# Performance work log

Measured on AMD Instinct MI355X. Metric: run time of the kernel, lower is better.

The kernel has to match this reference:

```python
import jax, jax.numpy as jnp
import numpy as np

B, N, C, Q, H, RATIO = 8, 8700, 256, 300, 8, 4
D = C // H
HID = C * RATIO
EPS = 1e-5


def _ln(x, w, b):
    m = jnp.mean(x, axis=-1, keepdims=True)
    v = jnp.mean((x - m) ** 2, axis=-1, keepdims=True)
    return (x - m) * jax.lax.rsqrt(v + EPS) * w + b


def setup_inputs() -> dict:
    key = jax.random.key(0)
    ks = jax.random.split(key, 8)
    s = 0.02
    return {
        "x": jax.random.normal(ks[0], (B, N, C), jnp.float32),
        # linear weights stored [in, out] (y = x @ W), no biases (qkv_bias=False, Mlp bias=False)
        "Wq": jax.random.normal(ks[1], (C, C), jnp.float32) * s,
        "Wk": jax.random.normal(ks[2], (C, C), jnp.float32) * s,
        "Wv": jax.random.normal(ks[3], (C, C), jnp.float32) * s,
        "Wp": jax.random.normal(ks[4], (C, C), jnp.float32) * s,
        "W1": jax.random.normal(ks[5], (C, HID), jnp.float32) * s,
        "W2": jax.random.normal(ks[6], (HID, C), jnp.float32) * s,
        "ln1_w": jnp.ones((C,), jnp.float32),
        "ln1_b": jnp.zeros((C,), jnp.float32),
        "ln2_w": jnp.ones((C,), jnp.float32),
        "ln2_b": jnp.zeros((C,), jnp.float32),
        "gamma1": jnp.ones((C,), jnp.float32),
        "gamma2": jnp.ones((C,), jnp.float32),
    }


def reference(x, Wq, Wk, Wv, Wp, W1, W2, ln1_w, ln1_b, ln2_w, ln2_b, gamma1, gamma2):
    scale = D ** -0.5
    xn = _ln(x, ln1_w, ln1_b)                       # [B,N,C]
    # SAQAttn: queries only from the first Q tokens; keys/values from all N tokens
    q = (xn[:, :Q] @ Wq).reshape(B, Q, H, D) * scale  # [B,Q,H,D]
    k = (xn @ Wk).reshape(B, N, H, D)
    v = (xn @ Wv).reshape(B, N, H, D)
    attn = jax.nn.softmax(jnp.einsum('bqhd,bnhd->bhqn', q, k), axis=-1)  # [B,H,Q,N]
    x_det = jnp.einsum('bhqn,bnhd->bqhd', attn, v).reshape(B, Q, C) @ Wp  # [B,Q,C]
    # residual with layer-scale gamma1; context tokens pass normed features through
    x_attn = jnp.concatenate([x_det, xn[:, Q:]], axis=1)
    x = x + gamma1 * x_attn
    # tokens_norm=False: norm2 only on query tokens
    x = jnp.concatenate([_ln(x[:, :Q], ln2_w, ln2_b), x[:, Q:]], axis=1)
    # MLP on query tokens with layer-scale gamma2 (exact GELU, as nn.GELU default)
    det = gamma2 * (jax.nn.gelu(x[:, :Q] @ W1, approximate=False) @ W2)
    # faithful to source: x_res + cat([det, x[:,Q:]]) doubles the context tokens
    return x + jnp.concatenate([det, x[:, Q:]], axis=1)
```

## Files before the change

kernel.cpp:

```cpp
#include <hip/hip_runtime.h>

#define BB 8
#define NN 8700
#define CC 256
#define QQ 300
#define HH 8
#define DD 32
#define HIDN 1024
#define NSPLIT 16
#define TSTR (NSPLIT * 64)
#define KSLACK 1536

typedef unsigned short u16;
typedef __attribute__((ext_vector_type(8))) short short8;
typedef __attribute__((ext_vector_type(4))) float f32x4;

#define MFMA16(a, b, c) __builtin_amdgcn_mfma_f32_16x16x32_bf16((a), (b), (c), 0, 0, 0)

__device__ __forceinline__ unsigned int cvtpk(float lo, float hi) {
    unsigned int r;
    asm("v_cvt_pk_bf16_f32 %0, %1, %2" : "=v"(r) : "v"(lo), "v"(hi));
    return r;
}
__device__ __forceinline__ u16 f2b_hw(float f) { return (u16)cvtpk(f, 0.f); }
__device__ __forceinline__ float b2f(u16 u) {
    unsigned int x = ((unsigned int)u) << 16;
    return __builtin_bit_cast(float, x);
}
__device__ __forceinline__ void gload16(const u16* g, u16* l) {
    __builtin_amdgcn_global_load_lds(
        (const __attribute__((address_space(1))) void*)g,
        (__attribute__((address_space(3))) void*)l, 16, 0, 0);
}

__global__ __launch_bounds__(256)
void wprep_t(const float* __restrict__ Wq, const float* __restrict__ Wk,
             const float* __restrict__ Wv, const float* __restrict__ Wp,
             const float* __restrict__ W1, const float* __restrict__ W2,
             u16* __restrict__ dst, float qscale)
{
    __shared__ u16 tl[64][66];
    int bid = blockIdx.x;
    const float* src; int K, N, tr, tc; size_t dof; float sc = 1.f;
    if (bid < 64) {
        int mat = bid >> 4, ti = bid & 15;
        src = (mat == 0) ? Wq : (mat == 1) ? Wk : (mat == 2) ? Wv : Wp;
        K = 256; N = 256; tr = ti >> 2; tc = ti & 3;
        dof = (size_t)mat * 65536;
        if (mat == 0) sc = qscale;
    } else if (bid < 128) {
        int ti = bid - 64; src = W1; K = 256; N = 1024; tr = ti >> 4; tc = ti & 15; dof = 262144;
    } else {
        int ti = bid - 128; src = W2; K = 1024; N = 256; tr = ti >> 2; tc = ti & 3; dof = 524288;
    }
    int tid = threadIdx.x;
    int jj = tid & 63;
    int i0 = tid >> 6;
#pragma unroll
    for (int ii = 0; ii < 16; ii++) {
        int kk = i0 * 16 + ii;
        float v = src[(size_t)(tr * 64 + kk) * N + tc * 64 + jj] * sc;
        tl[kk][jj] = f2b_hw(v);
    }
    __syncthreads();
#pragma unroll
    for (int ii = 0; ii < 16; ii++) {
        int nn = i0 * 16 + ii;
        dst[dof + (size_t)(tc * 64 + nn) * K + tr * 64 + jj] = tl[jj][nn];
    }
}

__global__ __launch_bounds__(256)
void ln1_k(const float* __restrict__ x, const float* __restrict__ w,
           const float* __restrict__ bv, const float* __restrict__ g1,
           u16* __restrict__ xn, float* __restrict__ out)
{
    int row = blockIdx.x * 4 + (threadIdx.x >> 6);
    int l = threadIdx.x & 63;
    size_t base = (size_t)row * CC + l * 4;
    float4 xv = *reinterpret_cast<const float4*>(x + base);
    float s  = xv.x + xv.y + xv.z + xv.w;
    float s2 = xv.x * xv.x + xv.y * xv.y + xv.z * xv.z + xv.w * xv.w;
#pragma unroll
    for (int m = 1; m < 64; m <<= 1) {
        s  += __shfl_xor(s,  m, 64);
        s2 += __shfl_xor(s2, m, 64);
    }
    float mean = s * (1.0f / CC);
    float rs = rsqrtf(s2 * (1.0f / CC) - mean * mean + 1e-5f);
    float4 wv = *reinterpret_cast<const float4*>(w  + l * 4);
    float4 bb = *reinterpret_cast<const float4*>(bv + l * 4);
    float n0 = (xv.x - mean) * rs * wv.x + bb.x;
    float n1 = (xv.y - mean) * rs * wv.y + bb.y;
    float n2 = (xv.z - mean) * rs * wv.z + bb.z;
    float n3 = (xv.w - mean) * rs * wv.w + bb.w;
    uint2 u; u.x = cvtpk(n0, n1); u.y = cvtpk(n2, n3);
    *reinterpret_cast<uint2*>(xn + base) = u;
    int n = row % NN;
    if (n >= QQ) {
        float4 gv = *reinterpret_cast<const float4*>(g1 + l * 4);
        float4 o;
        o.x = 2.0f * (xv.x + gv.x * n0);
        o.y = 2.0f * (xv.y + gv.y * n1);
        o.z = 2.0f * (xv.z + gv.z * n2);
        o.w = 2.0f * (xv.w + gv.w * n3);
        *reinterpret_cast<float4*>(out + base) = o;
    }
}

__global__ __launch_bounds__(256)
void ln2_k(const float* __restrict__ x, const float* __restrict__ pd,
           const float* __restrict__ g1, const float* __restrict__ w,
           const float* __restrict__ bv, float* __restrict__ xqf, u16* __restrict__ xqb)
{
    int r = blockIdx.x * 4 + (threadIdx.x >> 6);
    int l = threadIdx.x & 63;
    int b = r / QQ, n = r - b * QQ;
    size_t xoff = ((size_t)b * NN + n) * CC + l * 4;
    size_t roff = (size_t)r * CC + l * 4;
    float4 xv = *reinterpret_cast<const float4*>(x + xoff);
    float4 pv = *reinterpret_cast<const float4*>(pd + roff);
    float4 gv = *reinterpret_cast<const float4*>(g1 + l * 4);
    float x0 = xv.x + gv.x * pv.x;
    float x1 = xv.y + gv.y * pv.y;
    float x2 = xv.z + gv.z * pv.z;
    float x3 = xv.w + gv.w * pv.w;
    float s  = x0 + x1 + x2 + x3;
    float s2 = x0 * x0 + x1 * x1 + x2 * x2 + x3 * x3;
#pragma unroll
    for (int m = 1; m < 64; m <<= 1) {
        s  += __shfl_xor(s,  m, 64);
        s2 += __shfl_xor(s2, m, 64);
    }
    float mean = s * (1.0f / CC);
    float rs = rsqrtf(s2 * (1.0f / CC) - mean * mean + 1e-5f);
    float4 wv = *reinterpret_cast<const float4*>(w  + l * 4);
    float4 bb = *reinterpret_cast<const float4*>(bv + l * 4);
    float n0 = (x0 - mean) * rs * wv.x + bb.x;
    float n1 = (x1 - mean) * rs * wv.y + bb.y;
    float n2 = (x2 - mean) * rs * wv.z + bb.z;
    float n3 = (x3 - mean) * rs * wv.w + bb.w;
    float4 o; o.x = n0; o.y = n1; o.z = n2; o.w = n3;
    *reinterpret_cast<float4*>(xqf + roff) = o;
    uint2 u; u.x = cvtpk(n0, n1); u.y = cvtpk(n2, n3);
    *reinterpret_cast<uint2*>(xqb + roff) = u;
}

__global__ __launch_bounds__(512)
void gemm_kv(const u16* __restrict__ A, const u16* __restrict__ WT,
             u16* __restrict__ Cb, u16* __restrict__ Cb2, int M)
{
    __shared__ u16 alds[64 * 256];
    const int tid = threadIdx.x;
    const int w = tid >> 6, l = tid & 63;
    const int l15 = l & 15, kg = l >> 4;
    const int rowbase = blockIdx.x * 64;
    const f32x4 fz = {0.f, 0.f, 0.f, 0.f};

    {
        const char* gb = (const char*)(A + (size_t)rowbase * CC);
        char* lb = (char*)alds;
#pragma unroll
        for (int j = 0; j < 4; j++) {
            int o = tid * 64 + j * 16;
            short8 v = *reinterpret_cast<const short8*>(gb + o);
            int d = o ^ (((o >> 9) & 7) << 4);
            *reinterpret_cast<short8*>(lb + d) = v;
        }
    }
    __syncthreads();

    const int colbase = w * 64;
    const u16* bp[4];
#pragma unroll
    for (int ni = 0; ni < 4; ni++)
        bp[ni] = WT + (size_t)(colbase + ni * 16 + l15) * CC + kg * 8;

    f32x4 acc[4][4];
#pragma unroll
    for (int mi = 0; mi < 4; mi++)
#pragma unroll
        for (int ni = 0; ni < 4; ni++) acc[mi][ni] = fz;

    const char* lb = (const char*)alds;
    const int sw = (l15 & 7) << 4;
    int abase[4];
#pragma unroll
    for (int mi = 0; mi < 4; mi++) abase[mi] = (mi * 16 + l15) << 9;

#pragma unroll
    for (int ks = 0; ks < 8; ks++) {
        const int koff = ((ks * 64) + (kg * 16)) ^ sw;
        short8 a[4], bfr[4];
#pragma unroll
        for (int mi = 0; mi < 4; mi++)
            a[mi] = *reinterpret_cast<const short8*>(lb + abase[mi] + koff);
#pragma unroll
        for (int ni = 0; ni < 4; ni++)
            bfr[ni] = *reinterpret_cast<const short8*>(bp[ni] + ks * 32);
#pragma unroll
        for (int mi = 0; mi < 4; mi++)
#pragma unroll
            for (int ni = 0; ni < 4; ni++)
                acc[mi][ni] = MFMA16(bfr[ni], a[mi], acc[mi][ni]);
    }

#pragma unroll
    for (int mi = 0; mi < 4; mi++) {
        int r = rowbase + mi * 16 + l15;
        if (r >= M) continue;
#pragma unroll
        for (int ni = 0; ni < 4; ni++) {
            int col0 = colbase + ni * 16 + kg * 4;
            f32x4 v = acc[mi][ni];
            uint2 pk; pk.x = cvtpk(v[0], v[1]); pk.y = cvtpk(v[2], v[3]);
            if (col0 < CC) *reinterpret_cast<uint2*>(Cb  + (size_t)r * CC + col0)        = pk;
            else           *reinterpret_cast<uint2*>(Cb2 + (size_t)r * CC + (col0 - CC)) = pk;
        }
    }
}

template<int EPI, int MT>
__global__ __launch_bounds__(256)
void gemm_k(const u16* __restrict__ A, const u16* __restrict__ WT,
            u16* __restrict__ Cb, u16* __restrict__ Cb2, float* __restrict__ Cf,
            const float* __restrict__ basep, const float* __restrict__ gvec,
            float* __restrict__ outp,
            int M, int K, int ldC, int rpb, int bstr)
{
    constexpr int NM = MT / 16;
    const int w = threadIdx.x >> 6, l = threadIdx.x & 63;
    const int l15 = l & 15, kg = l >> 4;
    const int rowbase = blockIdx.x * MT;
    const int colbase = blockIdx.y * 256 + w * 64;
    const short8 z8 = {0, 0, 0, 0, 0, 0, 0, 0};
    const f32x4 fz = {0.f, 0.f, 0.f, 0.f};

    const u16* ap[NM]; bool av[NM];
#pragma unroll
    for (int mi = 0; mi < NM; mi++) {
        int r = rowbase + mi * 16 + l15;
        av[mi] = (r < M);
        int rr = av[mi] ? r : 0;
        size_t ar = (size_t)(rr / rpb) * bstr + (rr % rpb);
        ap[mi] = A + ar * K + kg * 8;
    }
    const u16* bp[4];
#pragma unroll
    for (int ni = 0; ni < 4; ni++) {
        int col = colbase + ni * 16 + l15;
        bp[ni] = WT + (size_t)col * K + kg * 8;
    }
    f32x4 acc[NM][4];
#pragma unroll
    for (int mi = 0; mi < NM; mi++)
#pragma unroll
        for (int ni = 0; ni < 4; ni++) acc[mi][ni] = fz;

    for (int ks = 0; ks < K; ks += 32) {
        short8 a[NM], bfr[4];
#pragma unroll
        for (int mi = 0; mi < NM; mi++)
            a[mi] = av[mi] ? *reinterpret_cast<const short8*>(ap[mi] + ks) : z8;
#pragma unroll
        for (int ni = 0; ni < 4; ni++)
            bfr[ni] = *reinterpret_cast<const short8*>(bp[ni] + ks);
#pragma unroll
        for (int mi = 0; mi < NM; mi++)
#pragma unroll
            for (int ni = 0; ni < 4; ni++)
                acc[mi][ni] = MFMA16(bfr[ni], a[mi], acc[mi][ni]);
    }
#pragma unroll
    for (int mi = 0; mi < NM; mi++) {
        int r = rowbase + mi * 16 + l15;
        if (r >= M) continue;
#pragma unroll
        for (int ni = 0; ni < 4; ni++) {
            int col0 = colbase + ni * 16 + kg * 4;
            f32x4 v = acc[mi][ni];
            if (EPI == 0) {
                uint2 pk; pk.x = cvtpk(v[0], v[1]); pk.y = cvtpk(v[2], v[3]);
                if (col0 < CC) *reinterpret_cast<uint2*>(Cb  + (size_t)r * ldC + col0)        = pk;
                else           *reinterpret_cast<uint2*>(Cb2 + (size_t)r * ldC + (col0 - CC)) = pk;
            } else if (EPI == 1) {
                float g0 = 0.5f * v[0] * (1.0f + erff(v[0] * 0.70710678118654752f));
                float g1 = 0.5f * v[1] * (1.0f + erff(v[1] * 0.70710678118654752f));
                float g2 = 0.5f * v[2] * (1.0f + erff(v[2] * 0.70710678118654752f));
                float g3 = 0.5f * v[3] * (1.0f + erff(v[3] * 0.70710678118654752f));
                uint2 pk; pk.x = cvtpk(g0, g1); pk.y = cvtpk(g2, g3);
                *reinterpret_cast<uint2*>(Cb + (size_t)r * ldC + col0) = pk;
            } else if (EPI == 2) {
                float4 o; o.x = v[0]; o.y = v[1]; o.z = v[2]; o.w = v[3];
                *reinterpret_cast<float4*>(Cf + (size_t)r * ldC + col0) = o;
            } else {
                float4 xv = *reinterpret_cast<const float4*>(basep + (size_t)r * CC + col0);
                float4 gv = *reinterpret_cast<const float4*>(gvec + col0);
                float4 o;
                o.x = xv.x + gv.x * v[0];
                o.y = xv.y + gv.y * v[1];
                o.z = xv.z + gv.z * v[2];
                o.w = xv.w + gv.w * v[3];
                size_t orow = (size_t)(r / QQ) * NN + (r % QQ);
                *reinterpret_cast<float4*>(outp + orow * CC + col0) = o;
            }
        }
    }
}

__global__ __launch_bounds__(256)
void attn_k(const u16* __restrict__ qm, const u16* __restrict__ km,
            const u16* __restrict__ vm, u16* __restrict__ Opb,
            float* __restrict__ lp)
{
    __shared__ u16 klds[2][64 * 32];
    __shared__ u16 vt[2][32 * 64];
    __shared__ u16 plds[4][2][16 * 64];

    const int bx = blockIdx.x;
    const int split = bx >> 6;
    const int rem = bx & 63;
    const int h = rem >> 3, b = rem & 7;
    const int bh = b * HH + h;
    const int tid = threadIdx.x;
    const int w = tid >> 6, l = tid & 63;
    const int l15 = l & 15, kg = l >> 4;
    const int tstart = split * 64;
    const int nt = (NN - tstart + TSTR - 1) / TSTR;

    const f32x4 fz = {0.f, 0.f, 0.f, 0.f};
    const short os = (short)0x3F80;
    const short8 ones = {os, os, os, os, os, os, os, os};

    const u16* kbase = km + (size_t)b * NN * CC + h * DD;
    const u16* vbase = vm + (size_t)b * NN * CC + h * DD;
    const int vkp = (tid & 31) * 2;
    const int vdg = (tid >> 5) * 4;

    const int krow  = (w << 4) + (l >> 2);
    const int kslot = (l & 3) ^ ((krow >> 1) & 3);
    const u16* ksrc = kbase + (size_t)krow * CC + kslot * 8;

    short8 qfr[5];
#pragma unroll
    for (int qf = 0; qf < 5; qf++) {
        int qrow = w * 80 + qf * 16 + l15;
        int qc = qrow < QQ ? qrow : 0;
        qfr[qf] = *reinterpret_cast<const short8*>(qm + ((size_t)(b * QQ + qc) * CC + h * DD + kg * 8));
    }

    f32x4 o[2][5]; float lpart[5];
#pragma unroll
    for (int qf = 0; qf < 5; qf++) { o[0][qf] = fz; o[1][qf] = fz; lpart[qf] = 0.f; }

    gload16(ksrc + (size_t)tstart * CC, (u16*)((char*)klds[0] + (w << 10)));
    ushort4 v0r = *reinterpret_cast<const ushort4*>(vbase + (size_t)(tstart + vkp) * CC + vdg);
    ushort4 v1r = *reinterpret_cast<const ushort4*>(vbase + (size_t)(tstart + vkp + 1) * CC + vdg);

    char* pl = (char*)plds[w];
    const int rdswz = ((l15 << 7) ^ ((l15 & 7) << 4)) + (kg << 4);
    const int wrbase = (l15 << 7) ^ ((l15 & 7) << 4);

    for (int t = 0; t < nt; ++t) {
        const int n0 = tstart + t * TSTR;
        char* vtb = (char*)vt[t & 1];
#pragma unroll
        for (int i = 0; i < 4; i++) {
            int row = vdg + i;
            unsigned int pk2 = (unsigned int)v0r[i] | ((unsigned int)v1r[i] << 16);
            int byteo = ((row << 7) + (vkp << 1)) ^ ((row & 7) << 4);
            *reinterpret_cast<unsigned int*>(vtb + byteo) = pk2;
        }
        __syncthreads();

        gload16(ksrc + (size_t)(n0 + TSTR) * CC, (u16*)((char*)klds[(t + 1) & 1] + (w << 10)));
        ushort4 v0n = *reinterpret_cast<const ushort4*>(vbase + (size_t)(n0 + TSTR + vkp) * CC + vdg);
        ushort4 v1n = *reinterpret_cast<const ushort4*>(vbase + (size_t)(n0 + TSTR + vkp + 1) * CC + vdg);

        short8 kf[4];
        { const char* klb = (const char*)klds[t & 1];
#pragma unroll
          for (int kb = 0; kb < 4; kb++) {
              int row = kb * 16 + l15;
              int off = (row << 6) + ((kg ^ ((row >> 1) & 3)) << 4);
              kf[kb] = *reinterpret_cast<const short8*>(klb + off);
          } }

        short8 va[2][2];
#pragma unroll
        for (int ks = 0; ks < 2; ks++)
#pragma unroll
            for (int dg = 0; dg < 2; dg++) {
                int row = dg * 16 + l15;
                int byteo = ((row << 7) + 64 * ks + 16 * kg) ^ ((row & 7) << 4);
                va[ks][dg] = *reinterpret_cast<const short8*>(vtb + byteo);
            }

        const bool tail = (n0 + 64 > NN);

#pragma unroll
        for (int qf = 0; qf < 5; qf++) {
            short8 bp0, bp1;
            if (qf > 0) {
                const char* plr = pl + (((qf - 1) & 1) << 11);
                bp0 = *reinterpret_cast<const short8*>(plr + rdswz);
                bp1 = *reinterpret_cast<const short8*>(plr + rdswz + 64);
            }
            f32x4 s[4];
            __builtin_amdgcn_s_setprio(1);
#pragma unroll
            for (int kb = 0; kb < 4; kb++)
                s[kb] = MFMA16(kf[kb], qfr[qf], fz);
            __builtin_amdgcn_s_setprio(0);
            char* plw = pl + ((qf & 1) << 11);
#pragma unroll
            for (int kb = 0; kb < 4; kb++) {
                float p0 = exp2f(s[kb][0]);
                float p1 = exp2f(s[kb][1]);
                float p2 = exp2f(s[kb][2]);
                float p3 = exp2f(s[kb][3]);
                if (tail) {
                    int kbase2 = n0 + 16 * kb + 4 * kg;
                    if (kbase2 + 0 >= NN) p0 = 0.f;
                    if (kbase2 + 1 >= NN) p1 = 0.f;
                    if (kbase2 + 2 >= NN) p2 = 0.f;
                    if (kbase2 + 3 >= NN) p3 = 0.f;
                }
                uint2 pw; pw.x = cvtpk(p0, p1); pw.y = cvtpk(p2, p3);
                *reinterpret_cast<uint2*>(plw + (wrbase + ((16 * kb + 4 * kg) << 1))) = pw;
            }
            if (qf > 0) {
                __builtin_amdgcn_s_setprio(1);
                o[0][qf - 1] = MFMA16(va[0][0], bp0, o[0][qf - 1]);
                o[1][qf - 1] = MFMA16(va[0][1], bp0, o[1][qf - 1]);
                o[0][qf - 1] = MFMA16(va[1][0], bp1, o[0][qf - 1]);
                o[1][qf - 1] = MFMA16(va[1][1], bp1, o[1][qf - 1]);
                f32x4 tsum = MFMA16(ones, bp0, fz);
                tsum = MFMA16(ones, bp1, tsum);
                __builtin_amdgcn_s_setprio(0);
                lpart[qf - 1] += tsum[0];
            }
        }
        {
            const char* plr = pl + 0;
            short8 bp0 = *reinterpret_cast<const short8*>(plr + rdswz);
            short8 bp1 = *reinterpret_cast<const short8*>(plr + rdswz + 64);
            __builtin_amdgcn_s_setprio(1);
            o[0][4] = MFMA16(va[0][0], bp0, o[0][4]);
            o[1][4] = MFMA16(va[0][1], bp0, o[1][4]);
            o[0][4] = MFMA16(va[1][0], bp1, o[0][4]);
            o[1][4] = MFMA16(va[1][1], bp1, o[1][4]);
            f32x4 tsum = MFMA16(ones, bp0, fz);
            tsum = MFMA16(ones, bp1, tsum);
            __builtin_amdgcn_s_setprio(0);
            lpart[4] += tsum[0];
        }
        v0r = v0n; v1r = v1n;
    }

    size_t pb = (size_t)(split * 64 + bh) * QQ;
#pragma unroll
    for (int qf = 0; qf < 5; qf++) {
        int q = w * 80 + qf * 16 + l15;
        if (q >= QQ) continue;
        size_t pr = pb + q;
        if (kg == 0) lp[pr] = lpart[qf];
        uint2 w0; w0.x = cvtpk(o[0][qf][0], o[0][qf][1]); w0.y = cvtpk(o[0][qf][2], o[0][qf][3]);
        uint2 w1; w1.x = cvtpk(o[1][qf][0], o[1][qf][1]); w1.y = cvtpk(o[1][qf][2], o[1][qf][3]);
        *reinterpret_cast<uint2*>(Opb + pr * DD + kg * 4)      = w0;
        *reinterpret_cast<uint2*>(Opb + pr * DD + 16 + kg * 4) = w1;
    }
}

__global__ __launch_bounds__(256)
void comb_k(const u16* __restrict__ Opb, const float* __restrict__ lp, u16* __restrict__ ao)
{
    int g = blockIdx.x * 256 + threadIdx.x;
    int d4 = (g & 7) * 4;
    int row = g >> 3;
    int bh = row / QQ, qq = row - bh * QQ;
    int b = bh >> 3, h = bh & 7;
    float L = 0.f, a0 = 0.f, a1 = 0.f, a2 = 0.f, a3 = 0.f;
#pragma unroll
    for (int s = 0; s < NSPLIT; s++) {
        size_t pr = (size_t)(s * 64 + bh) * QQ + qq;
        L += lp[pr];
        ushort4 ov = *reinterpret_cast<const ushort4*>(Opb + pr * DD + d4);
        a0 += b2f(ov.x); a1 += b2f(ov.y); a2 += b2f(ov.z); a3 += b2f(ov.w);
    }
    float inv = 1.0f / L;
    uint2 u; u.x = cvtpk(a0 * inv, a1 * inv); u.y = cvtpk(a2 * inv, a3 * inv);
    *reinterpret_cast<uint2*>(ao + ((size_t)(b * QQ + qq) * CC + h * DD + d4)) = u;
}

extern "C" void kernel_launch(void* const* d_in, const int* in_sizes, int n_in,
                              void* d_out, int out_size, void* d_ws, size_t ws_size,
                              hipStream_t stream)
{
    (void)in_sizes; (void)n_in; (void)out_size; (void)ws_size;
    const float* x    = (const float*)d_in[0];
    const float* Wq   = (const float*)d_in[1];
    const float* Wk   = (const float*)d_in[2];
    const float* Wv   = (const float*)d_in[3];
    const float* Wp   = (const float*)d_in[4];
    const float* W1   = (const float*)d_in[5];
    const float* W2   = (const float*)d_in[6];
    const float* ln1w = (const float*)d_in[7];
    const float* ln1b = (const float*)d_in[8];
    const float* ln2w = (const float*)d_in[9];
    const float* ln2b = (const float*)d_in[10];
    const float* g1   = (const float*)d_in[11];
    const float* g2   = (const float*)d_in[12];
    float* out = (float*)d_out;

    char* p = (char*)d_ws;
    auto alloc = [&](size_t bytes) { char* r = p; p += (bytes + 255) & ~(size_t)255; return r; };

    const size_t MKV = (size_t)BB * NN;
    const size_t MQ  = (size_t)BB * QQ;

    u16* WqT  = (u16*)alloc((size_t)CC * CC * 2);
    u16* WkvT = (u16*)alloc((size_t)CC * CC * 2 * 2);
    u16* WpT  = (u16*)alloc((size_t)CC * CC * 2);
    u16* W1T  = (u16*)alloc((size_t)CC * HIDN * 2);
    u16* W2T  = (u16*)alloc((size_t)HIDN * CC * 2);
    u16* xn   = (u16*)alloc((MKV + 64) * CC * 2);
    u16* kbf  = (u16*)alloc((MKV + KSLACK) * CC * 2);
    u16* vbf  = (u16*)alloc((MKV + KSLACK) * CC * 2);
    u16* qbf  = (u16*)alloc(MQ * CC * 2);
    u16* aob  = (u16*)alloc(MQ * CC * 2);
    u16* xqb  = (u16*)alloc(MQ * CC * 2);
    u16* h1   = (u16*)alloc(MQ * HIDN * 2);
    float* pd  = (float*)alloc(MQ * CC * 4);
    float* xqf = (float*)alloc(MQ * CC * 4);
    u16* Opb  = (u16*)alloc((size_t)NSPLIT * 64 * QQ * DD * 2);
    float* lp  = (float*)alloc((size_t)NSPLIT * 64 * QQ * 4);

    const float qscale = 0.17677669529663687f * 1.4426950408889634f;

    wprep_t<<<192, 256, 0, stream>>>(Wq, Wk, Wv, Wp, W1, W2, WqT, qscale);

    ln1_k<<<(int)(MKV / 4), 256, 0, stream>>>(x, ln1w, ln1b, g1, xn, out);

    gemm_kv<<<1088, 512, 0, stream>>>(xn, WkvT, kbf, vbf, (int)MKV);
    gemm_k<0, 16><<<dim3(150, 1), 256, 0, stream>>>(xn, WqT, qbf, nullptr, nullptr, nullptr, nullptr, nullptr,
                                                    (int)MQ, CC, CC, QQ, NN);

    attn_k<<<64 * NSPLIT, 256, 0, stream>>>(qbf, kbf, vbf, Opb, lp);
    comb_k<<<(int)(MQ * 8 / 256), 256, 0, stream>>>(Opb, lp, aob);

    gemm_k<2, 16><<<dim3(150, 1), 256, 0, stream>>>(aob, WpT, nullptr, nullptr, pd, nullptr, nullptr, nullptr,
                                                    (int)MQ, CC, CC, (int)MQ, 0);
    ln2_k<<<(int)(MQ / 4), 256, 0, stream>>>(x, pd, g1, ln2w, ln2b, xqf, xqb);

    gemm_k<1, 16><<<dim3(150, 4), 256, 0, stream>>>(xqb, W1T, h1, nullptr, nullptr, nullptr, nullptr, nullptr,
                                                    (int)MQ, CC, HIDN, (int)MQ, 0);
    gemm_k<3, 16><<<dim3(150, 1), 256, 0, stream>>>(h1, W2T, nullptr, nullptr, nullptr, xqf, g2, out,
                                                    (int)MQ, HIDN, CC, (int)MQ, 0);
}
```

Baseline: 223.4 us.

## Fuse LN1 with weight prep, and combine+proj+LN2 and the MLP into single kernels

LN1 and the weight transpose/convert now run as one launch. The split-attention combine, output projection, residual and LN2 are merged into one kernel that stages intermediates in LDS. The two MLP GEMMs with GELU are merged so the hidden activations stay in shared memory instead of going through global memory. This cuts launch count and intermediate global traffic. The cost is less parallelism: the MLP uses only 150 blocks, each computing the full hidden layer.

```diff
diff --git a/kernel.cpp b/kernel.cpp
--- a/kernel.cpp
+++ b/kernel.cpp
@@ -34,116 +34,77 @@
 }
 
 __global__ __launch_bounds__(256)
-void wprep_t(const float* __restrict__ Wq, const float* __restrict__ Wk,
-             const float* __restrict__ Wv, const float* __restrict__ Wp,
-             const float* __restrict__ W1, const float* __restrict__ W2,
-             u16* __restrict__ dst, float qscale)
+void prep_k(const float* __restrict__ x, const float* __restrict__ ln1w,
+            const float* __restrict__ ln1b, const float* __restrict__ g1,
+            u16* __restrict__ xn, float* __restrict__ out,
+            const float* __restrict__ Wq, const float* __restrict__ Wk,
+            const float* __restrict__ Wv, const float* __restrict__ Wp,
+            const float* __restrict__ W1, const float* __restrict__ W2,
+            u16* __restrict__ wdst, float qscale)
 {
     __shared__ u16 tl[64][66];
-    int bid = blockIdx.x;
-    const float* src; int K, N, tr, tc; size_t dof; float sc = 1.f;
-    if (bid < 64) {
-        int mat = bid >> 4, ti = bid & 15;
-        src = (mat == 0) ? Wq : (mat == 1) ? Wk : (mat == 2) ? Wv : Wp;
-        K = 256; N = 256; tr = ti >> 2; tc = ti & 3;
-        dof = (size_t)mat * 65536;
-        if (mat == 0) sc = qscale;
-    } else if (bid < 128) {
-        int ti = bid - 64; src = W1; K = 256; N = 1024; tr = ti >> 4; tc = ti & 15; dof = 262144;
+    if (blockIdx.x < 17400) {
+        int row = blockIdx.x * 4 + (threadIdx.x >> 6);
+        int l = threadIdx.x & 63;
+        size_t base = (size_t)row * CC + l * 4;
+        float4 xv = *reinterpret_cast<const float4*>(x + base);
+        float s  = xv.x + xv.y + xv.z + xv.w;
+        float s2 = xv.x * xv.x + xv.y * xv.y + xv.z * xv.z + xv.w * xv.w;
+#pragma unroll
+        for (int m = 1; m < 64; m <<= 1) {
+            s  += __shfl_xor(s,  m, 64);
+            s2 += __shfl_xor(s2, m, 64);
+        }
+        float mean = s * (1.0f / CC);
+        float rs = rsqrtf(s2 * (1.0f / CC) - mean * mean + 1e-5f);
+        float4 wv = *reinterpret_cast<const float4*>(ln1w + l * 4);
+        float4 bb = *reinterpret_cast<const float4*>(ln1b + l * 4);
+        float n0 = (xv.x - mean) * rs * wv.x + bb.x;
+        float n1 = (xv.y - mean) * rs * wv.y + bb.y;
+        float n2 = (xv.z - mean) * rs * wv.z + bb.z;
+        float n3 = (xv.w - mean) * rs * wv.w + bb.w;
+        uint2 u; u.x = cvtpk(n0, n1); u.y = cvtpk(n2, n3);
+        *reinterpret_cast<uint2*>(xn + base) = u;
+        int n = row % NN;
+        if (n >= QQ) {
+            float4 gv = *reinterpret_cast<const float4*>(g1 + l * 4);
+            float4 o;
+            o.x = 2.0f * (xv.x + gv.x * n0);
+            o.y = 2.0f * (xv.y + gv.y * n1);
+            o.z = 2.0f * (xv.z + gv.z * n2);
+            o.w = 2.0f * (xv.w + gv.w * n3);
+            *reinterpret_cast<float4*>(out + base) = o;
+        }
     } else {
-        int ti = bid - 128; src = W2; K = 1024; N = 256; tr = ti >> 2; tc = ti & 3; dof = 524288;
-    }
-    int tid = threadIdx.x;
-    int jj = tid & 63;
-    int i0 = tid >> 6;
-#pragma unroll
-    for (int ii = 0; ii < 16; ii++) {
-        int kk = i0 * 16 + ii;
-        float v = src[(size_t)(tr * 64 + kk) * N + tc * 64 + jj] * sc;
-        tl[kk][jj] = f2b_hw(v);
-    }
-    __syncthreads();
-#pragma unroll
-    for (int ii = 0; ii < 16; ii++) {
-        int nn = i0 * 16 + ii;
-        dst[dof + (size_t)(tc * 64 + nn) * K + tr * 64 + jj] = tl[jj][nn];
-    }
-}
-
-__global__ __launch_bounds__(256)
-void ln1_k(const float* __restrict__ x, const float* __restrict__ w,
-           const float* __restrict__ bv, const float* __restrict__ g1,
-           u16* __restrict__ xn, float* __restrict__ out)
-{
-    int row = blockIdx.x * 4 + (threadIdx.x >> 6);
-    int l = threadIdx.x & 63;
-    size_t base = (size_t)row * CC + l * 4;
-    float4 xv = *reinterpret_cast<const float4*>(x + base);
-    float s  = xv.x + xv.y + xv.z + xv.w;
-    float s2 = xv.x * xv.x + xv.y * xv.y + xv.z * xv.z + xv.w * xv.w;
-#pragma unroll
-    for (int m = 1; m < 64; m <<= 1) {
-        s  += __shfl_xor(s,  m, 64);
-        s2 += __shfl_xor(s2, m, 64);
-    }
-    float mean = s * (1.0f / CC);
-    float rs = rsqrtf(s2 * (1.0f / CC) - mean * mean + 1e-5f);
-    float4 wv = *reinterpret_cast<const float4*>(w  + l * 4);
-    float4 bb = *reinterpret_cast<const float4*>(bv + l * 4);
-    float n0 = (xv.x - mean) * rs * wv.x + bb.x;
-    float n1 = (xv.y - mean) * rs * wv.y + bb.y;
-    float n2 = (xv.z - mean) * rs * wv.z + bb.z;
-    float n3 = (xv.w - mean) * rs * wv.w + bb.w;
-    uint2 u; u.x = cvtpk(n0, n1); u.y = cvtpk(n2, n3);
-    *reinterpret_cast<uint2*>(xn + base) = u;
-    int n = row % NN;
-    if (n >= QQ) {
-        float4 gv = *reinterpret_cast<const float4*>(g1 + l * 4);
-        float4 o;
-        o.x = 2.0f * (xv.x + gv.x * n0);
-        o.y = 2.0f * (xv.y + gv.y * n1);
-        o.z = 2.0f * (xv.z + gv.z * n2);
-        o.w = 2.0f * (xv.w + gv.w * n3);
-        *reinterpret_cast<float4*>(out + base) = o;
-    }
-}
-
-__global__ __launch_bounds__(256)
-void ln2_k(const float* __restrict__ x, const float* __restrict__ pd,
-           const float* __restrict__ g1, const float* __restrict__ w,
-           const float* __restrict__ bv, float* __restrict__ xqf, u16* __restrict__ xqb)
-{
-    int r = blockIdx.x * 4 + (threadIdx.x >> 6);
-    int l = threadIdx.x & 63;
-    int b = r / QQ, n = r - b * QQ;
-    size_t xoff = ((size_t)b * NN + n) * CC + l * 4;
-    size_t roff = (size_t)r * CC + l * 4;
-    float4 xv = *reinterpret_cast<const float4*>(x + xoff);
-    float4 pv = *reinterpret_cast<const float4*>(pd + roff);
-    float4 gv = *reinterpret_cast<const float4*>(g1 + l * 4);
-    float x0 = xv.x + gv.x * pv.x;
-    float x1 = xv.y + gv.y * pv.y;
-    float x2 = xv.z + gv.z * pv.z;
-    float x3 = xv.w + gv.w * pv.w;
-    float s  = x0 + x1 + x2 + x3;
-    float s2 = x0 * x0 + x1 * x1 + x2 * x2 + x3 * x3;
-#pragma unroll
-    for (int m = 1; m < 64; m <<= 1) {
-        s  += __shfl_xor(s,  m, 64);
-        s2 += __shfl_xor(s2, m, 64);
-    }
-    float mean = s * (1.0f / CC);
-    float rs = rsqrtf(s2 * (1.0f / CC) - mean * mean + 1e-5f);
-    float4 wv = *reinterpret_cast<const float4*>(w  + l * 4);
-    float4 bb = *reinterpret_cast<const float4*>(bv + l * 4);
-    float n0 = (x0 - mean) * rs * wv.x + bb.x;
-    float n1 = (x1 - mean) * rs * wv.y + bb.y;
-    float n2 = (x2 - mean) * rs * wv.z + bb.z;
-    float n3 = (x3 - mean) * rs * wv.w + bb.w;
-    float4 o; o.x = n0; o.y = n1; o.z = n2; o.w = n3;
-    *reinterpret_cast<float4*>(xqf + roff) = o;
-    uint2 u; u.x = cvtpk(n0, n1); u.y = cvtpk(n2, n3);
-    *reinterpret_cast<uint2*>(xqb + roff) = u;
+        int bid = blockIdx.x - 17400;
+        const float* src; int K, N, tr, tc; size_t dof; float sc = 1.f;
+        if (bid < 64) {
+            int mat = bid >> 4, ti = bid & 15;
+            src = (mat == 0) ? Wq : (mat == 1) ? Wk : (mat == 2) ? Wv : Wp;
+            K = 256; N = 256; tr = ti >> 2; tc = ti & 3;
+            dof = (size_t)mat * 65536;
+            if (mat == 0) sc = qscale;
+        } else if (bid < 128) {
+            int ti = bid - 64; src = W1; K = 256; N = 1024; tr = ti >> 4; tc = ti & 15; dof = 262144;
+        } else {
+            int ti = bid - 128; src = W2; K = 1024; N = 256; tr = ti >> 2; tc = ti & 3; dof = 524288;
+        }
+        int tid = threadIdx.x;
+        int jj = tid & 63;
+        int i0 = tid >> 6;
+#pragma unroll
+        for (int ii = 0; ii < 16; ii++) {
+            int kk = i0 * 16 + ii;
+            float v = src[(size_t)(tr * 64 + kk) * N + tc * 64 + jj] * sc;
+            tl[kk][jj] = f2b_hw(v);
+        }
+        __syncthreads();
+#pragma unroll
+        for (int ii = 0; ii < 16; ii++) {
+            int nn = i0 * 16 + ii;
+            wdst[dof + (size_t)(tc * 64 + nn) * K + tr * 64 + jj] = tl[jj][nn];
+        }
+    }
 }
 
 __global__ __launch_bounds__(512)
@@ -220,90 +181,43 @@
     }
 }
 
-template<int EPI, int MT>
 __global__ __launch_bounds__(256)
-void gemm_k(const u16* __restrict__ A, const u16* __restrict__ WT,
-            u16* __restrict__ Cb, u16* __restrict__ Cb2, float* __restrict__ Cf,
-            const float* __restrict__ basep, const float* __restrict__ gvec,
-            float* __restrict__ outp,
-            int M, int K, int ldC, int rpb, int bstr)
+void gemm_q(const u16* __restrict__ A, const u16* __restrict__ WT, u16* __restrict__ Cb, int M)
 {
-    constexpr int NM = MT / 16;
     const int w = threadIdx.x >> 6, l = threadIdx.x & 63;
     const int l15 = l & 15, kg = l >> 4;
-    const int rowbase = blockIdx.x * MT;
-    const int colbase = blockIdx.y * 256 + w * 64;
+    const int rowbase = blockIdx.x * 16;
+    const int colbase = w * 64;
     const short8 z8 = {0, 0, 0, 0, 0, 0, 0, 0};
     const f32x4 fz = {0.f, 0.f, 0.f, 0.f};
 
-    const u16* ap[NM]; bool av[NM];
-#pragma unroll
-    for (int mi = 0; mi < NM; mi++) {
-        int r = rowbase + mi * 16 + l15;
-        av[mi] = (r < M);
-        int rr = av[mi] ? r : 0;
-        size_t ar = (size_t)(rr / rpb) * bstr + (rr % rpb);
-        ap[mi] = A + ar * K + kg * 8;
-    }
+    int r = rowbase + l15;
+    bool av = (r < M);
+    int rr = av ? r : 0;
+    const u16* ap = A + ((size_t)(rr / QQ) * NN + (rr % QQ)) * CC + kg * 8;
     const u16* bp[4];
 #pragma unroll
-    for (int ni = 0; ni < 4; ni++) {
-        int col = colbase + ni * 16 + l15;
-        bp[ni] = WT + (size_t)col * K + kg * 8;
-    }
-    f32x4 acc[NM][4];
-#pragma unroll
-    for (int mi = 0; mi < NM; mi++)
-#pragma unroll
-        for (int ni = 0; ni < 4; ni++) acc[mi][ni] = fz;
-
-    for (int ks = 0; ks < K; ks += 32) {
-        short8 a[NM], bfr[4];
-#pragma unroll
-        for (int mi = 0; mi < NM; mi++)
-            a[mi] = av[mi] ? *reinterpret_cast<const short8*>(ap[mi] + ks) : z8;
-#pragma unroll
-        for (int ni = 0; ni < 4; ni++)
-            bfr[ni] = *reinterpret_cast<const short8*>(bp[ni] + ks);
-#pragma unroll
-        for (int mi = 0; mi < NM; mi++)
-#pragma unroll
-            for (int ni = 0; ni < 4; ni++)
-                acc[mi][ni] = MFMA16(bfr[ni], a[mi], acc[mi][ni]);
-    }
-#pragma unroll
-    for (int mi = 0; mi < NM; mi++) {
-        int r = rowbase + mi * 16 + l15;
-        if (r >= M) continue;
+    for (int ni = 0; ni < 4; ni++)
+        bp[ni] = WT + (size_t)(colbase + ni * 16 + l15) * CC + kg * 8;
+
+    f32x4 acc[4];
+#pragma unroll
+    for (int ni = 0; ni < 4; ni++) acc[ni] = fz;
+
+    for (int ks = 0; ks < CC; ks += 32) {
+        short8 a = av ? *reinterpret_cast<const short8*>(ap + ks) : z8;
+#pragma unroll
+        for (int ni = 0; ni < 4; ni++) {
+            short8 bfr = *reinterpret_cast<const short8*>(bp[ni] + ks);
+            acc[ni] = MFMA16(bfr, a, acc[ni]);
+        }
+    }
+    if (r < M) {
 #pragma unroll
         for (int ni = 0; ni < 4; ni++) {
             int col0 = colbase + ni * 16 + kg * 4;
-            f32x4 v = acc[mi][ni];
-            if (EPI == 0) {
-                uint2 pk; pk.x = cvtpk(v[0], v[1]); pk.y = cvtpk(v[2], v[3]);
-                if (col0 < CC) *reinterpret_cast<uint2*>(Cb  + (size_t)r * ldC + col0)        = pk;
-                else           *reinterpret_cast<uint2*>(Cb2 + (size_t)r * ldC + (col0 - CC)) = pk;
-            } else if (EPI == 1) {
-                float g0 = 0.5f * v[0] * (1.0f + erff(v[0] * 0.70710678118654752f));
-                float g1 = 0.5f * v[1] * (1.0f + erff(v[1] * 0.70710678118654752f));
-                float g2 = 0.5f * v[2] * (1.0f + erff(v[2] * 0.70710678118654752f));
-                float g3 = 0.5f * v[3] * (1.0f + erff(v[3] * 0.70710678118654752f));
-                uint2 pk; pk.x = cvtpk(g0, g1); pk.y = cvtpk(g2, g3);
-                *reinterpret_cast<uint2*>(Cb + (size_t)r * ldC + col0) = pk;
-            } else if (EPI == 2) {
-                float4 o; o.x = v[0]; o.y = v[1]; o.z = v[2]; o.w = v[3];
-                *reinterpret_cast<float4*>(Cf + (size_t)r * ldC + col0) = o;
-            } else {
-                float4 xv = *reinterpret_cast<const float4*>(basep + (size_t)r * CC + col0);
-                float4 gv = *reinterpret_cast<const float4*>(gvec + col0);
-                float4 o;
-                o.x = xv.x + gv.x * v[0];
-                o.y = xv.y + gv.y * v[1];
-                o.z = xv.z + gv.z * v[2];
-                o.w = xv.w + gv.w * v[3];
-                size_t orow = (size_t)(r / QQ) * NN + (r % QQ);
-                *reinterpret_cast<float4*>(outp + orow * CC + col0) = o;
-            }
+            uint2 pk; pk.x = cvtpk(acc[ni][0], acc[ni][1]); pk.y = cvtpk(acc[ni][2], acc[ni][3]);
+            *reinterpret_cast<uint2*>(Cb + (size_t)r * CC + col0) = pk;
         }
     }
 }
@@ -473,24 +387,212 @@
 }
 
 __global__ __launch_bounds__(256)
-void comb_k(const u16* __restrict__ Opb, const float* __restrict__ lp, u16* __restrict__ ao)
+void cpl_k(const u16* __restrict__ Opb, const float* __restrict__ lp,
+           const u16* __restrict__ WpT, const float* __restrict__ x,
+           const float* __restrict__ g1, const float* __restrict__ w2,
+           const float* __restrict__ b2, float* __restrict__ xqf, u16* __restrict__ xqb)
 {
-    int g = blockIdx.x * 256 + threadIdx.x;
-    int d4 = (g & 7) * 4;
-    int row = g >> 3;
-    int bh = row / QQ, qq = row - bh * QQ;
-    int b = bh >> 3, h = bh & 7;
-    float L = 0.f, a0 = 0.f, a1 = 0.f, a2 = 0.f, a3 = 0.f;
-#pragma unroll
-    for (int s = 0; s < NSPLIT; s++) {
-        size_t pr = (size_t)(s * 64 + bh) * QQ + qq;
-        L += lp[pr];
-        ushort4 ov = *reinterpret_cast<const ushort4*>(Opb + pr * DD + d4);
-        a0 += b2f(ov.x); a1 += b2f(ov.y); a2 += b2f(ov.z); a3 += b2f(ov.w);
-    }
-    float inv = 1.0f / L;
-    uint2 u; u.x = cvtpk(a0 * inv, a1 * inv); u.y = cvtpk(a2 * inv, a3 * inv);
-    *reinterpret_cast<uint2*>(ao + ((size_t)(b * QQ + qq) * CC + h * DD + d4)) = u;
+    __shared__ u16 albs[16 * 256];
+    __shared__ float pdl[16][260];
+
+    const int tid = threadIdx.x;
+    const int r0 = blockIdx.x * 16;
+
+    {
+        int row = tid >> 4, cg = tid & 15;
+        int r = r0 + row;
+        int b = r / QQ, q = r - b * QQ;
+        int h = cg >> 1;
+        int dbase = (cg & 1) * 16;
+        float acc[16];
+#pragma unroll
+        for (int j = 0; j < 16; j++) acc[j] = 0.f;
+        float L = 0.f;
+        for (int s = 0; s < NSPLIT; s++) {
+            size_t pr = ((size_t)(s * 64) + b * 8 + h) * QQ + q;
+            L += lp[pr];
+            short8 v0 = *reinterpret_cast<const short8*>(Opb + pr * DD + dbase);
+            short8 v1 = *reinterpret_cast<const short8*>(Opb + pr * DD + dbase + 8);
+#pragma unroll
+            for (int j = 0; j < 8; j++) {
+                acc[j]     += b2f((u16)v0[j]);
+                acc[8 + j] += b2f((u16)v1[j]);
+            }
+        }
+        float inv = 1.0f / L;
+        short8 o0, o1;
+#pragma unroll
+        for (int j = 0; j < 4; j++) {
+            unsigned int a = cvtpk(acc[2 * j] * inv, acc[2 * j + 1] * inv);
+            unsigned int bq = cvtpk(acc[8 + 2 * j] * inv, acc[9 + 2 * j] * inv);
+            o0[2 * j] = (short)(a & 0xffff); o0[2 * j + 1] = (short)(a >> 16);
+            o1[2 * j] = (short)(bq & 0xffff); o1[2 * j + 1] = (short)(bq >> 16);
+        }
+        char* lb = (char*)albs;
+        int byte0 = (row << 9) + (cg << 5);
+        *reinterpret_cast<short8*>(lb + ((byte0)      ^ ((row & 7) << 4))) = o0;
+        *reinterpret_cast<short8*>(lb + ((byte0 + 16) ^ ((row & 7) << 4))) = o1;
+    }
+    __syncthreads();
+
+    const int w = tid >> 6, l = tid & 63;
+    const int l15 = l & 15, kg = l >> 4;
+    {
+        const f32x4 fz = {0.f, 0.f, 0.f, 0.f};
+        const int colbase = w * 64;
+        const u16* bp[4];
+#pragma unroll
+        for (int ni = 0; ni < 4; ni++)
+            bp[ni] = WpT + (size_t)(colbase + ni * 16 + l15) * CC + kg * 8;
+        f32x4 acc[4];
+#pragma unroll
+        for (int ni = 0; ni < 4; ni++) acc[ni] = fz;
+        const char* lb = (const char*)albs;
+        const int arow = l15 << 9;
+        const int sw = (l15 & 7) << 4;
+#pragma unroll
+        for (int ks = 0; ks < 8; ks++) {
+            short8 a = *reinterpret_cast<const short8*>(lb + (arow + ((kg * 16 + ks * 64) ^ sw)));
+#pragma unroll
+            for (int ni = 0; ni < 4; ni++) {
+                short8 bfr = *reinterpret_cast<const short8*>(bp[ni] + ks * 32);
+                acc[ni] = MFMA16(bfr, a, acc[ni]);
+            }
+        }
+#pragma unroll
+        for (int ni = 0; ni < 4; ni++) {
+            float4 v; v.x = acc[ni][0]; v.y = acc[ni][1]; v.z = acc[ni][2]; v.w = acc[ni][3];
+            *reinterpret_cast<float4*>(&pdl[l15][colbase + ni * 16 + kg * 4]) = v;
+        }
+    }
+    __syncthreads();
+
+    {
+        int row = tid >> 4, cg = tid & 15;
+        int r = r0 + row;
+        int b = r / QQ, q = r - b * QQ;
+        size_t xoff = ((size_t)b * NN + q) * CC + cg * 16;
+        float val[16];
+        float s = 0.f, s2 = 0.f;
+#pragma unroll
+        for (int j4 = 0; j4 < 4; j4++) {
+            float4 xv = *reinterpret_cast<const float4*>(x + xoff + j4 * 4);
+            float4 gv = *reinterpret_cast<const float4*>(g1 + cg * 16 + j4 * 4);
+            int c = cg * 16 + j4 * 4;
+            val[j4 * 4 + 0] = xv.x + gv.x * pdl[row][c + 0];
+            val[j4 * 4 + 1] = xv.y + gv.y * pdl[row][c + 1];
+            val[j4 * 4 + 2] = xv.z + gv.z * pdl[row][c + 2];
+            val[j4 * 4 + 3] = xv.w + gv.w * pdl[row][c + 3];
+#pragma unroll
+            for (int j = 0; j < 4; j++) {
+                float v = val[j4 * 4 + j];
+                s += v; s2 += v * v;
+            }
+        }
+#pragma unroll
+        for (int m = 1; m < 16; m <<= 1) {
+            s  += __shfl_xor(s,  m, 64);
+            s2 += __shfl_xor(s2, m, 64);
+        }
+        float mean = s * (1.0f / CC);
+        float rs = rsqrtf(s2 * (1.0f / CC) - mean * mean + 1e-5f);
+        size_t roff = (size_t)r * CC + cg * 16;
+#pragma unroll
+        for (int j4 = 0; j4 < 4; j4++) {
+            int c = cg * 16 + j4 * 4;
+            float4 wv = *reinterpret_cast<const float4*>(w2 + c);
+            float4 bb = *reinterpret_cast<const float4*>(b2 + c);
+            float n0 = (val[j4 * 4 + 0] - mean) * rs * wv.x + bb.x;
+            float n1 = (val[j4 * 4 + 1] - mean) * rs * wv.y + bb.y;
+            float n2 = (val[j4 * 4 + 2] - mean) * rs * wv.z + bb.z;
+            float n3 = (val[j4 * 4 + 3] - mean) * rs * wv.w + bb.w;
+            float4 o; o.x = n0; o.y = n1; o.z = n2; o.w = n3;
+            *reinterpret_cast<float4*>(xqf + roff + j4 * 4) = o;
+            uint2 u; u.x = cvtpk(n0, n1); u.y = cvtpk(n2, n3);
+            *reinterpret_cast<uint2*>(xqb + roff + j4 * 4) = u;
+        }
+    }
+}
+
+__global__ __launch_bounds__(256)
+void mlp_k(const u16* __restrict__ xqb, const u16* __restrict__ W1T,
+           const u16* __restrict__ W2T, const float* __restrict__ xqf,
+           const float* __restrict__ g2, float* __restrict__ out)
+{
+    __shared__ u16 h1l[16 * 1024];
+
+    const int tid = threadIdx.x;
+    const int w = tid >> 6, l = tid & 63;
+    const int l15 = l & 15, kg = l >> 4;
+    const int r0 = blockIdx.x * 16;
+    const f32x4 fz = {0.f, 0.f, 0.f, 0.f};
+
+    {
+        const u16* ap = xqb + (size_t)(r0 + l15) * CC + kg * 8;
+        f32x4 acc[16];
+#pragma unroll
+        for (int ni = 0; ni < 16; ni++) acc[ni] = fz;
+#pragma unroll
+        for (int ks = 0; ks < 8; ks++) {
+            short8 a = *reinterpret_cast<const short8*>(ap + ks * 32);
+#pragma unroll
+            for (int ni = 0; ni < 16; ni++) {
+                const u16* bp = W1T + (size_t)(w * 256 + ni * 16 + l15) * CC + kg * 8 + ks * 32;
+                short8 bfr = *reinterpret_cast<const short8*>(bp);
+                acc[ni] = MFMA16(bfr, a, acc[ni]);
+            }
+        }
+        char* lb = (char*)h1l;
+        const int sw = (l15 & 7) << 4;
+#pragma unroll
+        for (int ni = 0; ni < 16; ni++) {
+            float g0 = 0.5f * acc[ni][0] * (1.0f + erff(acc[ni][0] * 0.70710678118654752f));
+            float g1v = 0.5f * acc[ni][1] * (1.0f + erff(acc[ni][1] * 0.70710678118654752f));
+            float g2v = 0.5f * acc[ni][2] * (1.0f + erff(acc[ni][2] * 0.70710678118654752f));
+            float g3 = 0.5f * acc[ni][3] * (1.0f + erff(acc[ni][3] * 0.70710678118654752f));
+            uint2 pk; pk.x = cvtpk(g0, g1v); pk.y = cvtpk(g2v, g3);
+            int byteo = (l15 << 11) + (((w * 256 + ni * 16 + kg * 4) << 1) ^ sw);
+            *reinterpret_cast<uint2*>(lb + byteo) = pk;
+        }
+    }
+    __syncthreads();
+
+    {
+        const int colbase = w * 64;
+        const u16* bp[4];
+#pragma unroll
+        for (int ni = 0; ni < 4; ni++)
+            bp[ni] = W2T + (size_t)(colbase + ni * 16 + l15) * HIDN + kg * 8;
+        f32x4 acc[4];
+#pragma unroll
+        for (int ni = 0; ni < 4; ni++) acc[ni] = fz;
+        const char* lb = (const char*)h1l;
+        const int arow = l15 << 11;
+        const int sw = (l15 & 7) << 4;
+#pragma unroll
+        for (int ks = 0; ks < 32; ks++) {
+            short8 a = *reinterpret_cast<const short8*>(lb + arow + (((kg * 8 + ks * 32) << 1) ^ sw));
+#pragma unroll
+            for (int ni = 0; ni < 4; ni++) {
+                short8 bfr = *reinterpret_cast<const short8*>(bp[ni] + ks * 32);
+                acc[ni] = MFMA16(bfr, a, acc[ni]);
+            }
+        }
+        int r = r0 + l15;
+        size_t orow = (size_t)(r / QQ) * NN + (r % QQ);
+#pragma unroll
+        for (int ni = 0; ni < 4; ni++) {
+            int col0 = colbase + ni * 16 + kg * 4;
+            float4 xv = *reinterpret_cast<const float4*>(xqf + (size_t)r * CC + col0);
+            float4 gv = *reinterpret_cast<const float4*>(g2 + col0);
+            float4 o;
+            o.x = xv.x + gv.x * acc[ni][0];
+            o.y = xv.y + gv.y * acc[ni][1];
+            o.z = xv.z + gv.z * acc[ni][2];
+            o.w = xv.w + gv.w * acc[ni][3];
+            *reinterpret_cast<float4*>(out + orow * CC + col0) = o;
+        }
+    }
 }
 
 extern "C" void kernel_launch(void* const* d_in, const int* in_sizes, int n_in,
@@ -528,33 +630,22 @@
     u16* kbf  = (u16*)alloc((MKV + KSLACK) * CC * 2);
     u16* vbf  = (u16*)alloc((MKV + KSLACK) * CC * 2);
     u16* qbf  = (u16*)alloc(MQ * CC * 2);
-    u16* aob  = (u16*)alloc(MQ * CC * 2);
     u16* xqb  = (u16*)alloc(MQ * CC * 2);
-    u16* h1   = (u16*)alloc(MQ * HIDN * 2);
-    float* pd  = (float*)alloc(MQ * CC * 4);
     float* xqf = (float*)alloc(MQ * CC * 4);
     u16* Opb  = (u16*)alloc((size_t)NSPLIT * 64 * QQ * DD * 2);
     float* lp  = (float*)alloc((size_t)NSPLIT * 64 * QQ * 4);
 
     const float qscale = 0.17677669529663687f * 1.4426950408889634f;
 
-    wprep_t<<<192, 256, 0, stream>>>(Wq, Wk, Wv, Wp, W1, W2, WqT, qscale);
-
-    ln1_k<<<(int)(MKV / 4), 256, 0, stream>>>(x, ln1w, ln1b, g1, xn, out);
+    prep_k<<<17592, 256, 0, stream>>>(x, ln1w, ln1b, g1, xn, out,
+                                      Wq, Wk, Wv, Wp, W1, W2, WqT, qscale);
 
     gemm_kv<<<1088, 512, 0, stream>>>(xn, WkvT, kbf, vbf, (int)MKV);
-    gemm_k<0, 16><<<dim3(150, 1), 256, 0, stream>>>(xn, WqT, qbf, nullptr, nullptr, nullptr, nullptr, nullptr,
-                                                    (int)MQ, CC, CC, QQ, NN);
+    gemm_q<<<150, 256, 0, stream>>>(xn, WqT, qbf, (int)MQ);
 
     attn_k<<<64 * NSPLIT, 256, 0, stream>>>(qbf, kbf, vbf, Opb, lp);
-    comb_k<<<(int)(MQ * 8 / 256), 256, 0, stream>>>(Opb, lp, aob);
-
-    gemm_k<2, 16><<<dim3(150, 1), 256, 0, stream>>>(aob, WpT, nullptr, nullptr, pd, nullptr, nullptr, nullptr,
-                                                    (int)MQ, CC, CC, (int)MQ, 0);
-    ln2_k<<<(int)(MQ / 4), 256, 0, stream>>>(x, pd, g1, ln2w, ln2b, xqf, xqb);
-
-    gemm_k<1, 16><<<dim3(150, 4), 256, 0, stream>>>(xqb, W1T, h1, nullptr, nullptr, nullptr, nullptr, nullptr,
-                                                    (int)MQ, CC, HIDN, (int)MQ, 0);
-    gemm_k<3, 16><<<dim3(150, 1), 256, 0, stream>>>(h1, W2T, nullptr, nullptr, nullptr, xqf, g2, out,
-                                                    (int)MQ, HIDN, CC, (int)MQ, 0);
-}
+
+    cpl_k<<<150, 256, 0, stream>>>(Opb, lp, WpT, x, g1, ln2w, ln2b, xqf, xqb);
+
+    mlp_k<<<150, 256, 0, stream>>>(xqb, W1T, W2T, xqf, g2, out);
+}
```

Result: no change. 225.2 us (+0.8%).
